# Kernel optimization log

Measured on AMD Instinct MI355X. Metric: run time of the kernel, lower is better.

## Reference

```python
import jax, jax.numpy as jnp
import numpy as np

K = 3            # kernel_size
S = 4            # up_factor
VMAX = 1.0
TAU = 0.5
CENTER_BIAS = 2.5
SMOOTH_RES = 0.15
C_IN = 21
HIDDEN = 48
B_, H0, W0 = 4, 81, 81
CTR = K // 2      # = 1, also GL recursion depth M


def _dir_step_diff(k):
    """Precompute (base_pos - base_neg) per direction/step: [8, M+1, k, k]."""
    c = k // 2
    dirs = np.array([[1, 0], [1, 1], [0, 1], [-1, 1], [-1, 0], [-1, -1], [0, -1], [1, -1]], np.float32)
    dirs = dirs / (np.linalg.norm(dirs, axis=1, keepdims=True) + 1e-8)
    yy, xx = np.meshgrid(np.arange(k), np.arange(k), indexing='ij')
    rel = np.stack([yy - c, xx - c], -1).astype(np.float32)
    diff = np.zeros((8, c + 1, k, k), np.float32)
    for d in range(8):
        v = dirs[d]
        proj = rel[..., 0] * v[1] + rel[..., 1] * v[0]
        step = np.clip(np.round(proj), -c, c).astype(np.int64)
        for m in range(c + 1):
            diff[d, m] = (step == m).astype(np.float32) - (step == -m).astype(np.float32)
    return diff

DIFF = jnp.asarray(_dir_step_diff(K))  # [8, M+1, K, K]


def conv3x3(x, w, b):
    y = jax.lax.conv_general_dilated(x, w, (1, 1), 'SAME',
                                     dimension_numbers=('NCHW', 'OIHW', 'NCHW'))
    return y + b[None, :, None, None]


def bilinear_up(x, s):
    """F.interpolate(scale_factor=s, mode='bilinear', align_corners=True)."""
    B, C, h, w = x.shape
    H, W = h * s, w * s
    ys = jnp.linspace(0.0, h - 1.0, H)
    xs = jnp.linspace(0.0, w - 1.0, W)
    y0 = jnp.clip(jnp.floor(ys).astype(jnp.int32), 0, h - 2)
    x0 = jnp.clip(jnp.floor(xs).astype(jnp.int32), 0, w - 2)
    wy = (ys - y0)[:, None]
    wx = (xs - x0)[None, :]
    x00 = x[:, :, y0][:, :, :, x0]
    x01 = x[:, :, y0][:, :, :, x0 + 1]
    x10 = x[:, :, y0 + 1][:, :, :, x0]
    x11 = x[:, :, y0 + 1][:, :, :, x0 + 1]
    return (x00 * (1 - wy) * (1 - wx) + x01 * (1 - wy) * wx
            + x10 * wy * (1 - wx) + x11 * wy * wx)


def setup_inputs() -> dict:
    key = jax.random.key(0)
    ks = jax.random.split(key, 6)
    wn = lambda k, shape: jax.random.normal(k, shape, jnp.float32) * 0.05
    return {
        'x': jax.random.normal(ks[0], (B_, C_IN, H0, W0), jnp.float32),
        'w1o': wn(ks[1], (HIDDEN, C_IN, 3, 3)), 'b1o': jnp.zeros((HIDDEN,), jnp.float32),
        'w2o': wn(ks[2], (8, HIDDEN, 3, 3)), 'b2o': jnp.zeros((8,), jnp.float32),
        'w1g': wn(ks[3], (HIDDEN, C_IN, 3, 3)), 'b1g': jnp.zeros((HIDDEN,), jnp.float32),
        'w2g': wn(ks[4], (1, HIDDEN, 3, 3)), 'b2g': jnp.zeros((1,), jnp.float32),
        'beta': jnp.asarray(1.6, jnp.float32),
    }


def reference(x, w1o, b1o, w2o, b2o, w1g, b1g, w2g, b2g, beta):
    B, C, h, w = x.shape
    c = CTR
    # heads
    raw_v = conv3x3(jax.nn.relu(conv3x3(x, w1o, b1o)), w2o, b2o)          # [B,8,h,w]
    g = jax.nn.sigmoid(conv3x3(jax.nn.relu(conv3x3(x, w1g, b1g)), w2g, b2g))  # [B,1,h,w]
    v = VMAX * jnp.tanh(raw_v)
    # Gruenwald-Letnikov coefficients, M = center (=1 for k=3)
    coeffs = [jnp.ones_like(v)]
    wm = coeffs[0]
    for m in range(1, c + 1):
        wm = wm * (v - m + 1.0) / m * -1.0
        coeffs.append(wm)
    coeff = jnp.stack(coeffs, axis=2)                                      # [B,8,M+1,h,w]
    # direction kernels, averaged over the 8 directions
    ker = jnp.einsum('bdmhw,dmkl->bklhw', coeff, DIFF) / 8.0               # [B,K,K,h,w]
    mask_pre = ker.reshape(B, K * K, h, w)
    ci = c * K + c
    # NOTE: torch adds center_bias in-place on a view of ker -> ker itself is biased too
    mask_pre = mask_pre.at[:, ci].add(CENTER_BIAS)
    ker_b = mask_pre.reshape(B, K, K, h, w)
    mask_lp = jax.nn.softmax(mask_pre / TAU, axis=1)                       # [B,9,h,w]
    # unfold 3x3 window with reflect padding
    xp = jnp.pad(x, ((0, 0), (0, 0), (c, c), (c, c)), mode='reflect')
    patches = jnp.stack([xp[:, :, i:i + h, j:j + w]
                         for i in range(K) for j in range(K)], axis=2)     # [B,C,9,h,w]
    rep2 = lambda a, ax: jnp.repeat(jnp.repeat(a, S, axis=ax), S, axis=ax + 1)
    neigh = rep2(patches, 3)                                               # [B,C,9,H,W]
    mask_lp_u = rep2(mask_lp, 2)                                           # [B,9,H,W]
    g_up = rep2(g, 2)                                                      # [B,1,H,W]
    x_up = bilinear_up(x, S)                                               # [B,C,H,W]
    y_lp_out = jnp.einsum('bcnHW,bnHW->bcHW', neigh, mask_lp_u)
    lam = SMOOTH_RES * (1.0 - g_up)
    y_lp = x_up + lam * (y_lp_out - x_up)
    # highpass branch (mode='both')
    ker_hp = ker_b - ker_b.mean(axis=(1, 2), keepdims=True)
    ker_hp = ker_hp / (jnp.abs(ker_hp).sum(axis=(1, 2), keepdims=True) + 1e-8)
    mask_hp = rep2(ker_hp.reshape(B, K * K, h, w), 2)
    y_hp = jnp.einsum('bcnHW,bnHW->bcHW', neigh, mask_hp)
    y = y_lp + jnp.tanh(beta) * g_up * y_hp
    return (y, v, g_up)
```

## Files before the change

kernel.cpp:

```cpp
#include <hip/hip_runtime.h>
#include <math.h>

#define B_N   4
#define CIN   21
#define HIDC  48
#define H0    81
#define NP    6561
#define HH    324
#define NPH   104976

__device__ __forceinline__ float tanh_fast(float x) {
    float e = __expf(2.f * x);
    return 1.f - 2.f / (e + 1.f);
}

__global__ __launch_bounds__(256) void k1_conv1(
    const float* __restrict__ x,
    const float* __restrict__ w1o, const float* __restrict__ b1o,
    const float* __restrict__ w1g, const float* __restrict__ b1g,
    float* __restrict__ hid_o, float* __restrict__ hid_g)
{
    __shared__ __align__(16) float wt[189 * 12];
    __shared__ float bs[12];
    const int tid = threadIdx.x;
    const int grp = blockIdx.y;
    const int b   = blockIdx.z;
    const bool head_o = (grp < 4);
    const int ocb = (grp & 3) * 12;
    const float* wsrc = head_o ? w1o : w1g;
    for (int i = tid; i < 189 * 12; i += 256) {
        const int ict = i / 12, oc = i - ict * 12;
        wt[i] = wsrc[(ocb + oc) * 189 + ict];
    }
    if (tid < 12) bs[tid] = (head_o ? b1o : b1g)[ocb + tid];
    __syncthreads();

    const int px = blockIdx.x * 256 + tid;
    const bool valid = (px < NP);
    const int oy = px / H0, ox = px - oy * H0;
    const float* xb = x + (size_t)b * CIN * NP;

    float acc[12];
    #pragma unroll
    for (int j = 0; j < 12; j++) acc[j] = bs[j];

    for (int ic = 0; ic < CIN; ic++) {
        const float* xc = xb + ic * NP;
        float xv[9];
        #pragma unroll
        for (int ky = 0; ky < 3; ky++) {
            const int iy = oy + ky - 1;
            const bool rok = valid && ((unsigned)iy < (unsigned)H0);
            #pragma unroll
            for (int kx = 0; kx < 3; kx++) {
                const int ix = ox + kx - 1;
                const bool ok = rok && ((unsigned)ix < (unsigned)H0);
                xv[ky * 3 + kx] = ok ? xc[iy * H0 + ix] : 0.f;
            }
        }
        #pragma unroll
        for (int tap = 0; tap < 9; tap++) {
            const float4 w0 = *(const float4*)&wt[(ic * 9 + tap) * 12];
            const float4 w1 = *(const float4*)&wt[(ic * 9 + tap) * 12 + 4];
            const float4 w2 = *(const float4*)&wt[(ic * 9 + tap) * 12 + 8];
            const float wj[12] = {w0.x, w0.y, w0.z, w0.w, w1.x, w1.y, w1.z, w1.w,
                                  w2.x, w2.y, w2.z, w2.w};
            const float xvt = xv[tap];
            #pragma unroll
            for (int j = 0; j < 12; j++) acc[j] = fmaf(xvt, wj[j], acc[j]);
        }
    }

    if (valid) {
        float* outp = (head_o ? hid_o : hid_g) + ((size_t)b * HIDC + ocb) * NP + px;
        #pragma unroll
        for (int j = 0; j < 12; j++) outp[j * NP] = fmaxf(acc[j], 0.f);
    }
}

__global__ __launch_bounds__(256) void k2up(
    const float* __restrict__ x,
    const float* __restrict__ hid_o, const float* __restrict__ hid_g,
    const float* __restrict__ w2o, const float* __restrict__ b2o,
    const float* __restrict__ w2g, const float* __restrict__ b2g,
    const float* __restrict__ beta,
    float* __restrict__ v_out, float* __restrict__ y_out,
    float* __restrict__ gup_out)
{
    __shared__ __align__(16) float wo_s[HIDC * 9 * 8];
    __shared__ float wg_s[HIDC * 9];
    __shared__ float red[4][32][12];
    __shared__ float res_s[32][29];
    __shared__ float xs[CIN][4][H0];
    const int tid = threadIdx.x;
    const int b = blockIdx.y;

    const int pl  = tid & 31;
    const int s   = tid >> 5;
    const int w   = tid >> 6;
    const int px0 = blockIdx.x * 32;
    const int px  = px0 + pl;
    const bool valid = (px < NP);
    const int py  = px / H0, pxc = px - py * H0;
    const int pr0 = px0 / H0;

    {
        const float* xb = x + (size_t)b * CIN * NP;
        for (int i = tid; i < CIN * 4 * H0; i += 256) {
            const int c = i / (4 * H0), rem = i - c * (4 * H0);
            const int t = rem / H0, col = rem - t * H0;
            int r = pr0 - 1 + t;
            r = (r < 0) ? -r : r;
            r = (r > H0 - 1) ? 2 * (H0 - 1) - r : r;
            (&xs[0][0][0])[i] = xb[c * NP + r * H0 + col];
        }
    }

    for (int i = tid; i < HIDC * 9 * 8; i += 256) {
        const int d = i / (HIDC * 9), r = i - d * (HIDC * 9);
        wo_s[r * 8 + d] = w2o[i];
    }
    for (int i = tid; i < HIDC * 9; i += 256) wg_s[i] = w2g[i];
    __syncthreads();

    const int ic0 = s * 6;
    const float* po = hid_o + ((size_t)b * HIDC + ic0) * NP;
    const float* pg = hid_g + ((size_t)b * HIDC + ic0) * NP;

    float a[8] = {0.f, 0.f, 0.f, 0.f, 0.f, 0.f, 0.f, 0.f};
    float ag = 0.f;

    #pragma unroll 1
    for (int ky = 0; ky < 3; ky++) {
        const int iy = py + ky - 1;
        const bool rok = valid && ((unsigned)iy < (unsigned)H0);
        #pragma unroll
        for (int kx = 0; kx < 3; kx++) {
            const int ix = pxc + kx - 1;
            const bool ok = rok && ((unsigned)ix < (unsigned)H0);
            const int off = iy * H0 + ix;
            const int tap = ky * 3 + kx;
            #pragma unroll
            for (int j = 0; j < 6; j++) {
                const float vo = ok ? po[j * NP + off] : 0.f;
                const float vg = ok ? pg[j * NP + off] : 0.f;
                const int wb = ((ic0 + j) * 9 + tap) * 8;
                const float4 wA = *(const float4*)&wo_s[wb];
                const float4 wB = *(const float4*)&wo_s[wb + 4];
                a[0] = fmaf(vo, wA.x, a[0]); a[1] = fmaf(vo, wA.y, a[1]);
                a[2] = fmaf(vo, wA.z, a[2]); a[3] = fmaf(vo, wA.w, a[3]);
                a[4] = fmaf(vo, wB.x, a[4]); a[5] = fmaf(vo, wB.y, a[5]);
                a[6] = fmaf(vo, wB.z, a[6]); a[7] = fmaf(vo, wB.w, a[7]);
                ag = fmaf(vg, wg_s[(ic0 + j) * 9 + tap], ag);
            }
        }
    }

    #pragma unroll
    for (int n = 0; n < 8; n++) a[n] += __shfl_xor(a[n], 32);
    ag += __shfl_xor(ag, 32);
    if ((tid & 32) == 0) {
        #pragma unroll
        for (int n = 0; n < 8; n++) red[w][pl][n] = a[n];
        red[w][pl][8] = ag;
    }
    __syncthreads();

    if (tid < 32 && valid) {
        float v[8];
        #pragma unroll
        for (int n = 0; n < 8; n++)
            v[n] = tanh_fast(red[0][tid][n] + red[1][tid][n] + red[2][tid][n]
                             + red[3][tid][n] + b2o[n]);
        const float agf = red[0][tid][8] + red[1][tid][8] + red[2][tid][8]
                        + red[3][tid][8] + b2g[0];
        const float g = 1.f / (1.f + __expf(-agf));

        constexpr float DT[8][9] = {
            {-1, 0, 1, -1, 0, 1, -1, 0, 1},
            {-1,-1, 0, -1, 0, 1,  0, 1, 1},
            {-1,-1,-1,  0, 0, 0,  1, 1, 1},
            { 0,-1,-1,  1, 0,-1,  1, 1, 0},
            { 1, 0,-1,  1, 0,-1,  1, 0,-1},
            { 1, 1, 0,  1, 0,-1,  0,-1,-1},
            { 1, 1, 1,  0, 0, 0, -1,-1,-1},
            { 0, 1, 1, -1, 0, 1, -1,-1, 0}};
        float ker[9];
        #pragma unroll
        for (int n = 0; n < 9; n++) {
            float t = 0.f;
            #pragma unroll
            for (int d = 0; d < 8; d++) t += v[d] * DT[d][n];
            ker[n] = -0.125f * t;
        }
        ker[4] += 2.5f;
        float mx = ker[0];
        #pragma unroll
        for (int n = 1; n < 9; n++) mx = fmaxf(mx, ker[n]);
        float exn[9], sum = 0.f;
        #pragma unroll
        for (int n = 0; n < 9; n++) { exn[n] = __expf((ker[n] - mx) * 2.0f); sum += exn[n]; }
        const float rs = 1.f / sum;
        float mean = 0.f;
        #pragma unroll
        for (int n = 0; n < 9; n++) mean += ker[n];
        mean *= (1.f / 9.f);
        float den = 1e-8f;
        #pragma unroll
        for (int n = 0; n < 9; n++) den += fabsf(ker[n] - mean);
        const float rd = 1.f / den;

        #pragma unroll
        for (int n = 0; n < 8; n++) res_s[tid][n] = v[n];
        res_s[tid][8] = g;
        #pragma unroll
        for (int n = 0; n < 9; n++) {
            res_s[tid][9 + n]  = exn[n] * rs;
            res_s[tid][18 + n] = (ker[n] - mean) * rd;
        }
    }
    __syncthreads();

    if (valid) v_out[((size_t)b * 8 + s) * NP + px] = res_s[pl][s];

    const float tb = tanh_fast(beta[0]);
    for (int i = tid; i < 22 * 32; i += 256) {
        const int plane = i >> 5, pp = i & 31;
        const int p = px0 + pp;
        if (p >= NP) continue;
        const int ppy = p / H0, ppx = p - ppy * H0;
        const float gv = res_s[pp][8];

        if (plane == 21) {
            float* gdst = gup_out + (size_t)b * NPH;
            #pragma unroll
            for (int dh = 0; dh < 4; dh++)
                *reinterpret_cast<float4*>(gdst + (size_t)(ppy * 4 + dh) * HH + ppx * 4) =
                    make_float4(gv, gv, gv, gv);
            continue;
        }

        const int d0 = ppy - pr0;
        const int xm = (ppx == 0) ? 1 : ppx - 1;
        const int xp = (ppx == H0 - 1) ? H0 - 2 : ppx + 1;
        float w9[9];
        #pragma unroll
        for (int t = 0; t < 3; t++) {
            w9[t * 3 + 0] = xs[plane][d0 + t][xm];
            w9[t * 3 + 1] = xs[plane][d0 + t][ppx];
            w9[t * 3 + 2] = xs[plane][d0 + t][xp];
        }

        float alp = 0.f, ahp = 0.f;
        #pragma unroll
        for (int t = 0; t < 9; t++) {
            alp = fmaf(w9[t], res_s[pp][9 + t],  alp);
            ahp = fmaf(w9[t], res_s[pp][18 + t], ahp);
        }

        const float lam = 0.15f * (1.f - gv);
        const float gh  = tb * gv;

        int sxv[4]; float wxv[4];
        #pragma unroll
        for (int k = 0; k < 4; k++) {
            const int W = ppx * 4 + k;
            const float xsf = (float)W * (80.f / 323.f);
            int x0 = (int)xsf;
            if (x0 > H0 - 2) x0 = H0 - 2;
            wxv[k] = xsf - (float)x0;
            sxv[k] = x0 - ppx + 1;
        }

        float* ydst = y_out + ((size_t)b * CIN + plane) * NPH;
        #pragma unroll
        for (int dh = 0; dh < 4; dh++) {
            const int H = ppy * 4 + dh;
            const float ysf = (float)H * (80.f / 323.f);
            int y0 = (int)ysf;
            if (y0 > H0 - 2) y0 = H0 - 2;
            const float wy = ysf - (float)y0;
            const int sy = y0 - ppy + 1;
            const float A0 = sy ? w9[3] : w9[0];
            const float A1 = sy ? w9[4] : w9[1];
            const float A2 = sy ? w9[5] : w9[2];
            const float B0 = sy ? w9[6] : w9[3];
            const float B1 = sy ? w9[7] : w9[4];
            const float B2 = sy ? w9[8] : w9[5];
            float rr[4];
            #pragma unroll
            for (int k = 0; k < 4; k++) {
                const float wx = wxv[k];
                const float top = sxv[k] ? fmaf(A2 - A1, wx, A1) : fmaf(A1 - A0, wx, A0);
                const float bot = sxv[k] ? fmaf(B2 - B1, wx, B1) : fmaf(B1 - B0, wx, B0);
                const float xup = fmaf(bot - top, wy, top);
                rr[k] = fmaf(lam, alp - xup, xup) + gh * ahp;
            }
            *reinterpret_cast<float4*>(ydst + (size_t)H * HH + ppx * 4) =
                make_float4(rr[0], rr[1], rr[2], rr[3]);
        }
    }
}

extern "C" void kernel_launch(void* const* d_in, const int* in_sizes, int n_in,
                              void* d_out, int out_size, void* d_ws, size_t ws_size,
                              hipStream_t stream)
{
    const float* x    = (const float*)d_in[0];
    const float* w1o  = (const float*)d_in[1];
    const float* b1o  = (const float*)d_in[2];
    const float* w2o  = (const float*)d_in[3];
    const float* b2o  = (const float*)d_in[4];
    const float* w1g  = (const float*)d_in[5];
    const float* b1g  = (const float*)d_in[6];
    const float* w2g  = (const float*)d_in[7];
    const float* b2g  = (const float*)d_in[8];
    const float* beta = (const float*)d_in[9];
    float* out = (float*)d_out;
    float* wsf = (float*)d_ws;

    float* hid_o = wsf;
    float* hid_g = hid_o + (size_t)B_N * HIDC * NP;

    float* y_out = out;
    float* v_out = out + (size_t)B_N * CIN * NPH;
    float* gup   = v_out + (size_t)B_N * 8 * NP;

    k1_conv1<<<dim3((NP + 255) / 256, 8, B_N), 256, 0, stream>>>(
        x, w1o, b1o, w1g, b1g, hid_o, hid_g);
    k2up<<<dim3((NP + 31) / 32, B_N), 256, 0, stream>>>(
        x, hid_o, hid_g, w2o, b2o, w2g, b2g, beta, v_out, y_out, gup);
}
```

Measured before the change: 144.3 us.

## Tile k2up by row segments and stage hidden-O halo in shared memory

Remaps the second kernel from flat 32-pixel chunks to a (column tile, row, batch) grid. Each block now handles 32 columns of one row, which lets it stage a 3-row by 34-column halo of the 48-channel hid_o tensor in shared memory and read the 3x3 taps from there instead of global memory. The x halo buffer shrinks to the same 3x34 window with reflect indexing. The cost is 3 column tiles per row with the last only partly used (81 of 96 lanes active) and extra shared memory, which may lower occupancy. The hid_g taps still come from global memory.

```diff
diff --git a/kernel.cpp b/kernel.cpp
--- a/kernel.cpp
+++ b/kernel.cpp
@@ -12,6 +12,11 @@
 __device__ __forceinline__ float tanh_fast(float x) {
     float e = __expf(2.f * x);
     return 1.f - 2.f / (e + 1.f);
+}
+
+__device__ __forceinline__ int reflect81(int v) {
+    v = (v < 0) ? -v : v;
+    return (v > H0 - 1) ? 2 * (H0 - 1) - v : v;
 }
 
 __global__ __launch_bounds__(256) void k1_conv1(
@@ -89,42 +94,51 @@
 {
     __shared__ __align__(16) float wo_s[HIDC * 9 * 8];
     __shared__ float wg_s[HIDC * 9];
-    __shared__ float red[4][32][12];
+    __shared__ float red[4][32][9];
     __shared__ float res_s[32][29];
-    __shared__ float xs[CIN][4][H0];
+    __shared__ float hid_s[HIDC][3][34];
+    __shared__ float xs[CIN][3][34];
     const int tid = threadIdx.x;
-    const int b = blockIdx.y;
+    const int ct  = blockIdx.x;
+    const int r   = blockIdx.y;
+    const int b   = blockIdx.z;
+    const int c0  = ct * 32;
 
     const int pl  = tid & 31;
     const int s   = tid >> 5;
     const int w   = tid >> 6;
-    const int px0 = blockIdx.x * 32;
-    const int px  = px0 + pl;
-    const bool valid = (px < NP);
-    const int py  = px / H0, pxc = px - py * H0;
-    const int pr0 = px0 / H0;
-
+    const bool valid = (c0 + pl < H0);
+    const int pxc = c0 + pl;
+    const int px  = r * H0 + pxc;
+
+    {
+        const float* hb = hid_o + (size_t)b * HIDC * NP;
+        for (int i = tid; i < HIDC * 3 * 34; i += 256) {
+            const int ch = i / 102, rem = i - ch * 102;
+            const int ky = rem / 34, j = rem - ky * 34;
+            const int gr = r - 1 + ky, gc = c0 - 1 + j;
+            const bool ok = ((unsigned)gr < (unsigned)H0) && ((unsigned)gc < (unsigned)H0);
+            hid_s[ch][ky][j] = ok ? hb[ch * NP + gr * H0 + gc] : 0.f;
+        }
+    }
     {
         const float* xb = x + (size_t)b * CIN * NP;
-        for (int i = tid; i < CIN * 4 * H0; i += 256) {
-            const int c = i / (4 * H0), rem = i - c * (4 * H0);
-            const int t = rem / H0, col = rem - t * H0;
-            int r = pr0 - 1 + t;
-            r = (r < 0) ? -r : r;
-            r = (r > H0 - 1) ? 2 * (H0 - 1) - r : r;
-            (&xs[0][0][0])[i] = xb[c * NP + r * H0 + col];
-        }
-    }
-
+        for (int i = tid; i < CIN * 3 * 34; i += 256) {
+            const int ch = i / 102, rem = i - ch * 102;
+            const int ky = rem / 34, j = rem - ky * 34;
+            const int gr = reflect81(r - 1 + ky);
+            const int gc = reflect81(c0 - 1 + j);
+            xs[ch][ky][j] = xb[ch * NP + gr * H0 + gc];
+        }
+    }
     for (int i = tid; i < HIDC * 9 * 8; i += 256) {
-        const int d = i / (HIDC * 9), r = i - d * (HIDC * 9);
-        wo_s[r * 8 + d] = w2o[i];
+        const int d = i / (HIDC * 9), rr = i - d * (HIDC * 9);
+        wo_s[rr * 8 + d] = w2o[i];
     }
     for (int i = tid; i < HIDC * 9; i += 256) wg_s[i] = w2g[i];
     __syncthreads();
 
     const int ic0 = s * 6;
-    const float* po = hid_o + ((size_t)b * HIDC + ic0) * NP;
     const float* pg = hid_g + ((size_t)b * HIDC + ic0) * NP;
 
     float a[8] = {0.f, 0.f, 0.f, 0.f, 0.f, 0.f, 0.f, 0.f};
@@ -132,7 +146,7 @@
 
     #pragma unroll 1
     for (int ky = 0; ky < 3; ky++) {
-        const int iy = py + ky - 1;
+        const int iy = r + ky - 1;
         const bool rok = valid && ((unsigned)iy < (unsigned)H0);
         #pragma unroll
         for (int kx = 0; kx < 3; kx++) {
@@ -142,7 +156,7 @@
             const int tap = ky * 3 + kx;
             #pragma unroll
             for (int j = 0; j < 6; j++) {
-                const float vo = ok ? po[j * NP + off] : 0.f;
+                const float vo = hid_s[ic0 + j][ky][pl + kx];
                 const float vg = ok ? pg[j * NP + off] : 0.f;
                 const int wb = ((ic0 + j) * 9 + tap) * 8;
                 const float4 wA = *(const float4*)&wo_s[wb];
@@ -226,29 +240,25 @@
     const float tb = tanh_fast(beta[0]);
     for (int i = tid; i < 22 * 32; i += 256) {
         const int plane = i >> 5, pp = i & 31;
-        const int p = px0 + pp;
-        if (p >= NP) continue;
-        const int ppy = p / H0, ppx = p - ppy * H0;
+        if (c0 + pp >= H0) continue;
+        const int ppx = c0 + pp;
         const float gv = res_s[pp][8];
 
         if (plane == 21) {
             float* gdst = gup_out + (size_t)b * NPH;
             #pragma unroll
             for (int dh = 0; dh < 4; dh++)
-                *reinterpret_cast<float4*>(gdst + (size_t)(ppy * 4 + dh) * HH + ppx * 4) =
+                *reinterpret_cast<float4*>(gdst + (size_t)(r * 4 + dh) * HH + ppx * 4) =
                     make_float4(gv, gv, gv, gv);
             continue;
         }
 
-        const int d0 = ppy - pr0;
-        const int xm = (ppx == 0) ? 1 : ppx - 1;
-        const int xp = (ppx == H0 - 1) ? H0 - 2 : ppx + 1;
         float w9[9];
         #pragma unroll
         for (int t = 0; t < 3; t++) {
-            w9[t * 3 + 0] = xs[plane][d0 + t][xm];
-            w9[t * 3 + 1] = xs[plane][d0 + t][ppx];
-            w9[t * 3 + 2] = xs[plane][d0 + t][xp];
+            w9[t * 3 + 0] = xs[plane][t][pp];
+            w9[t * 3 + 1] = xs[plane][t][pp + 1];
+            w9[t * 3 + 2] = xs[plane][t][pp + 2];
         }
 
         float alp = 0.f, ahp = 0.f;
@@ -275,12 +285,12 @@
         float* ydst = y_out + ((size_t)b * CIN + plane) * NPH;
         #pragma unroll
         for (int dh = 0; dh < 4; dh++) {
-            const int H = ppy * 4 + dh;
+            const int H = r * 4 + dh;
             const float ysf = (float)H * (80.f / 323.f);
             int y0 = (int)ysf;
             if (y0 > H0 - 2) y0 = H0 - 2;
             const float wy = ysf - (float)y0;
-            const int sy = y0 - ppy + 1;
+            const int sy = y0 - r + 1;
             const float A0 = sy ? w9[3] : w9[0];
             const float A1 = sy ? w9[4] : w9[1];
             const float A2 = sy ? w9[5] : w9[2];
@@ -328,6 +338,6 @@
 
     k1_conv1<<<dim3((NP + 255) / 256, 8, B_N), 256, 0, stream>>>(
         x, w1o, b1o, w1g, b1g, hid_o, hid_g);
-    k2up<<<dim3((NP + 31) / 32, B_N), 256, 0, stream>>>(
+    k2up<<<dim3(3, H0, B_N), 256, 0, stream>>>(
         x, hid_o, hid_g, w2o, b2o, w2g, b2g, beta, v_out, y_out, gup);
 }
```

After: 150.8 us. +4.5%, slower.
